# Performance work log

Hardware: AMD Instinct MI355X
Metric: run time of the kernel (lower is better)

## Reference

```python
import jax, jax.numpy as jnp
import numpy as np

N = 10000; E = 60000; D = 3000; H = 512; L = 128; P = 256
NUM_MASK = 3000  # int(0.3 * N)

def prelu(x, a):
    return jnp.where(x >= 0, x, a * x)

def setup_inputs() -> dict:
    key = jax.random.key(0)
    ks = jax.random.split(key, 32)
    def rn(k, shape, scale=0.02):
        return jax.random.normal(k, shape, jnp.float32) * scale
    inp = {
        'x': jax.random.normal(ks[0], (N, D), jnp.float32),
        'edge_index': jax.random.randint(ks[1], (2, E), 0, N),
        'perm': jax.random.permutation(ks[2], N),
        'shuffle': jax.random.permutation(ks[3], N - NUM_MASK),
        's_W1': rn(ks[4], (D, H)), 's_b1': jnp.zeros((H,), jnp.float32), 's_a': jnp.full((1,), 0.25, jnp.float32),
        's_W2': rn(ks[5], (H, L)), 's_b2': jnp.zeros((L,), jnp.float32),
        't_W1': rn(ks[6], (D, H)), 't_b1': jnp.zeros((H,), jnp.float32), 't_a': jnp.full((1,), 0.25, jnp.float32),
        't_W2': rn(ks[7], (H, L)), 't_b2': jnp.zeros((L,), jnp.float32),
        'p_W1': rn(ks[8], (L, P)), 'p_b1': jnp.zeros((P,), jnp.float32), 'p_a': jnp.full((1,), 0.25, jnp.float32),
        'p_W2': rn(ks[9], (P, L)), 'p_b2': jnp.zeros((L,), jnp.float32),
        'tp_W1': rn(ks[10], (L, P)), 'tp_b1': jnp.zeros((P,), jnp.float32), 'tp_a': jnp.full((1,), 0.25, jnp.float32),
        'tp_W2': rn(ks[11], (P, L)), 'tp_b2': jnp.zeros((L,), jnp.float32),
        'dgi_W': rn(ks[12], (L, L), 0.05),
        'pos_token': rn(ks[13], (1, D)), 'neg_token': rn(ks[14], (1, D)),
        'e2d_W': rn(ks[15], (L, L), 0.05),
        'd_W': rn(ks[16], (L, D)), 'd_b': jnp.zeros((D,), jnp.float32),
    }
    return inp

def reference(x, edge_index, perm, shuffle, s_W1, s_b1, s_a, s_W2, s_b2, t_W1, t_b1, t_a, t_W2, t_b2, p_W1, p_b1, p_a, p_W2, p_b2, tp_W1, tp_b1, tp_a, tp_W2, tp_b2, dgi_W, pos_token, neg_token, e2d_W, d_W, d_b):
    n = x.shape[0]
    # GCN normalization with added self loops (PyG gcn_norm, flow source->target)
    loops = jnp.arange(n)
    src = jnp.concatenate([edge_index[0], loops])
    dst = jnp.concatenate([edge_index[1], loops])
    deg = jax.ops.segment_sum(jnp.ones(dst.shape, x.dtype), dst, n)
    dinv = jnp.where(deg > 0, jax.lax.rsqrt(deg), 0.0)
    enorm = (dinv[src] * dinv[dst])[:, None]  # [E+N, 1]

    def gcn(h, W, b):
        h = h @ W  # transform first, then propagate (PyG GCNConv)
        return jax.ops.segment_sum(h[src] * enorm, dst, n) + b

    # feature masking / corruption (bn=False -> Identity; no dropout at eval)
    mask_nodes = perm[:NUM_MASK]
    keep_nodes = perm[NUM_MASK:]
    use_pos = x.at[mask_nodes].add(pos_token[0])
    use_neg = jnp.zeros_like(x).at[keep_nodes].set(x[keep_nodes][shuffle]).at[mask_nodes].add(neg_token[0])

    # student / teacher two-layer GCN encoders (shared PReLU param per encoder)
    rep_pos = prelu(gcn(prelu(gcn(use_pos, s_W1, s_b1), s_a), s_W2, s_b2), s_a)
    rep_neg = prelu(gcn(prelu(gcn(use_neg, t_W1, t_b1), t_a), t_W2, t_b2), t_a)

    def proj(z, W1, b1, a, W2, b2):
        return prelu(z @ W1 + b1, a) @ W2 + b2

    pos_z = proj(rep_pos[mask_nodes], p_W1, p_b1, p_a, p_W2, p_b2)
    neg_z = proj(rep_neg[mask_nodes], tp_W1, tp_b1, tp_a, tp_W2, tp_b2)

    # DGI loss with sigmoid summary of positive embeddings
    s = jax.nn.sigmoid(pos_z.mean(axis=0))  # [L]
    ws = dgi_W @ s
    pos_d = jax.nn.sigmoid(pos_z @ ws)
    neg_d = jax.nn.sigmoid(neg_z @ ws)
    dgi_loss = -jnp.log(pos_d + 1e-15).mean() - jnp.log(1.0 - neg_d + 1e-15).mean()

    # reconstruction: re-mask latent, single-GCN feature decoder (no activation)
    rec = (rep_pos @ e2d_W).at[mask_nodes].set(0.0)
    rec = gcn(rec, d_W, d_b)

    # SCE loss with alpha = 2
    def l2n(v):
        return v / jnp.maximum(jnp.linalg.norm(v, axis=-1, keepdims=True), 1e-12)
    cos = (l2n(x[mask_nodes]) * l2n(rec[mask_nodes])).sum(axis=-1)
    feat_loss = ((1.0 - cos) ** 2).mean()
    return (feat_loss, dgi_loss)
```

## Files before the change

### kernel.cpp

```cpp
#include <hip/hip_runtime.h>

#define NND 10000
#define EE  60000
#define DD  3000
#define HH  512
#define LL  128
#define PP  256
#define NM  3000

#define KP  3072
#define MP  10240
#define NW  1024
#define KTILES (KP/64)

#define BMT 320
#define BNT 128
#define AH_STR 10240
#define AB_STR 20480
#define BH_STR 4096
#define BB_STR 8192

typedef short bf16x8 __attribute__((ext_vector_type(8)));
typedef float f32x4 __attribute__((ext_vector_type(4)));

__device__ __align__(256) char g_ws[(size_t)176 << 20];

__device__ __forceinline__ unsigned short f2b(float f){
    unsigned int x = __float_as_uint(f);
    unsigned int r = x + 0x7FFFu + ((x >> 16) & 1u);
    return (unsigned short)(r >> 16);
}
__device__ __forceinline__ float b2f(unsigned short u){
    return __uint_as_float(((unsigned int)u) << 16);
}
__device__ __forceinline__ float2 bpair(unsigned int u){
    float2 r;
    r.x = __uint_as_float(u << 16);
    r.y = __uint_as_float(u & 0xffff0000u);
    return r;
}
__device__ __forceinline__ unsigned int packb(float a, float b){
    return (unsigned int)f2b(a) | ((unsigned int)f2b(b) << 16);
}

__device__ __forceinline__ void gl_lds16(const void* g, void* l){
    __builtin_amdgcn_global_load_lds(
        (const __attribute__((address_space(1))) unsigned int*)g,
        (__attribute__((address_space(3))) unsigned int*)l, 16, 0, 0);
}


__global__ void init_k(int* degi, int* cursor, float* scal,
                       float* ptW, float* ntW, float* svecraw, int* ecnt){
    int i = blockIdx.x*256 + threadIdx.x;
    if (i < NND){ degi[i]=0; cursor[i]=0; }
    if (i < 80) scal[i]=0.f;
    if (i == 0) ecnt[0]=0;
    if (i < 128) svecraw[i]=0.f;
    if (i < HH){ ptW[i]=0.f; ntW[i]=0.f; }
}

__global__ void count_k(const int* __restrict__ ei, int* degi){
    int i = blockIdx.x*256 + threadIdx.x;
    if (i < EE) atomicAdd(&degi[ei[EE + i]], 1);
}

__global__ void flag_k(const int* __restrict__ perm, const int* __restrict__ shuf,
                       int* flag, int* negsrc){
    int i = blockIdx.x*256 + threadIdx.x;
    if (i < NND){
        int p = perm[i];
        if (i < NM){ flag[p] = 1; negsrc[p] = -1; }
        else       { flag[p] = 0; negsrc[p] = perm[NM + shuf[i - NM]]; }
    }
}

__global__ __launch_bounds__(256) void alloc_k(const int* __restrict__ degi,
                                               float* dinv, int* rowptr, int* ecnt){
    __shared__ int sb[256];
    __shared__ int bbase;
    int t = threadIdx.x;
    int i = blockIdx.x*256 + t;
    int v = (i < NND) ? degi[i] : 0;
    sb[t] = v;
    __syncthreads();
    for (int off = 1; off < 256; off <<= 1){
        int x = 0;
        if (t >= off) x = sb[t - off];
        __syncthreads();
        sb[t] += x;
        __syncthreads();
    }
    if (t == 255) bbase = atomicAdd(ecnt, sb[255]);
    __syncthreads();
    if (i < NND){
        rowptr[i] = bbase + sb[t] - v;
        dinv[i] = 1.f/sqrtf((float)(degi[i] + 1));
    }
}

__global__ void fill_k(const int* __restrict__ ei, const int* __restrict__ rowptr,
                       int* cursor, int* adj){
    int i = blockIdx.x*256 + threadIdx.x;
    if (i < EE){
        int d = ei[EE + i];
        int s = ei[i];
        int p = atomicAdd(&cursor[d], 1);
        adj[rowptr[d] + p] = s;
    }
}

__global__ __launch_bounds__(512) void tok_k(const float* __restrict__ posT,
        const float* __restrict__ negT,
        const float* __restrict__ sW1, const float* __restrict__ tW1,
        float* ptW, float* ntW){
    int b = blockIdx.x; int chunk = blockIdx.y; int j = threadIdx.x;
    const float* tok = b ? negT : posT;
    const float* Wm  = b ? tW1  : sW1;
    float acc = 0.f;
    int d0 = chunk * (DD/8), d1 = d0 + (DD/8);
    for (int d = d0; d < d1; ++d) acc += tok[d] * Wm[(long)d*HH + j];
    atomicAdd(&((b ? ntW : ptW)[j]), acc);
}


__global__ __launch_bounds__(256) void cast_pad_x_k(const float* __restrict__ x,
                                                    unsigned short* __restrict__ xb){
    long idx = (long)blockIdx.x*256 + threadIdx.x;
    if (idx >= (long)MP*(KP/8)) return;
    int row = (int)(idx / (KP/8));
    int g   = (int)(idx % (KP/8));
    unsigned short o[8] = {0,0,0,0,0,0,0,0};
    if (row < NND && g < DD/8){
        const float* src = x + (long)row*DD + g*8;
        float4 a = *(const float4*)(src);
        float4 b = *(const float4*)(src + 4);
        o[0]=f2b(a.x); o[1]=f2b(a.y); o[2]=f2b(a.z); o[3]=f2b(a.w);
        o[4]=f2b(b.x); o[5]=f2b(b.y); o[6]=f2b(b.z); o[7]=f2b(b.w);
    }
    *(uint4*)(xb + (long)row*KP + g*8) = *(const uint4*)o;
}

struct TBatch {
    const float* in[10];
    unsigned short* out[10];
    int R[10], C[10], OS[10];
    int t0[11];
};

__global__ void transbatch_k(TBatch tb){
    __shared__ unsigned short tile[32][33];
    int b = blockIdx.x;
    int d = 0;
    while (d < 9 && b >= tb.t0[d+1]) d++;
    const float* in = tb.in[d];
    unsigned short* out = tb.out[d];
    int R = tb.R[d], C = tb.C[d], OS = tb.OS[d];
    int lt = b - tb.t0[d];
    int Ctiles = (C + 31) >> 5;
    int rt = lt / Ctiles, ct = lt % Ctiles;
    int rb = rt*32, cb = ct*32;
    int tx = threadIdx.x, ty = threadIdx.y;
    for (int i = ty; i < 32; i += 8){
        int r = rb + i, c = cb + tx;
        tile[i][tx] = (r < R && c < C) ? f2b(in[(long)r*C + c]) : (unsigned short)0;
    }
    __syncthreads();
    for (int i = ty; i < 32; i += 8){
        int c = cb + i, r = rb + tx;
        if (c < C && r < OS) out[(long)c*OS + r] = (r < R) ? tile[tx][i] : (unsigned short)0;
    }
}


#define LDA(PB, MT, KS) (*(const bf16x8*)&As[(PB) + (KS)*AH_STR + a_off + (MT)*512])
#define LDB(PB, NT, KS) (*(const bf16x8*)&Bs[(PB) + (KS)*BH_STR + b_off + (NT)*512])

#define STG_A(KT, PDST, P) gl_lds16(asrc[P] + ((KT)<<6), &As[(PDST) + adst[P]])
#define STG_B(KT, PDST, Q) gl_lds16(bsrc[Q] + ((KT)<<6), &Bs[(PDST) + bdst[Q]])

#define GATE7 asm volatile("s_waitcnt vmcnt(7)" ::: "memory")
#define GATE0 asm volatile("s_waitcnt vmcnt(0)" ::: "memory")
#define NOOPS ((void)0)
#define AFENCE asm volatile("" ::: "memory")
#define BARR  { AFENCE; __builtin_amdgcn_s_barrier(); AFENCE; }

#define TILE_BODY(S1_STMT, S2_STMT, GATE_STMT) {                                  \
    bf16x8 af_[5][2], bf_[4][2];                                                  \
    _Pragma("unroll") for (int nt = 0; nt < 4; ++nt){                             \
        bf_[nt][0] = LDB(pB, nt, 0); bf_[nt][1] = LDB(pB, nt, 1); }               \
    _Pragma("unroll") for (int mt = 0; mt < 5; ++mt){                             \
        af_[mt][0] = LDA(pA, mt, 0); af_[mt][1] = LDA(pA, mt, 1); }               \
    S1_STMT;                                                                      \
    BARR;                                                                         \
    __builtin_amdgcn_s_setprio(1);                                                \
    _Pragma("unroll") for (int ks = 0; ks < 2; ++ks)                              \
      _Pragma("unroll") for (int nt = 0; nt < 4; ++nt)                            \
        _Pragma("unroll") for (int mt = 0; mt < 2; ++mt)                          \
          acc[mt][nt] = __builtin_amdgcn_mfma_f32_16x16x32_bf16(af_[mt][ks], bf_[nt][ks], acc[mt][nt], 0,0,0); \
    __builtin_amdgcn_s_setprio(0);                                                \
    BARR;                                                                         \
    S2_STMT;                                                                      \
    __builtin_amdgcn_s_setprio(1);                                                \
    _Pragma("unroll") for (int ks = 0; ks < 2; ++ks)                              \
      _Pragma("unroll") for (int nt = 0; nt < 4; ++nt)                            \
        _Pragma("unroll") for (int mt = 2; mt < 5; ++mt)                          \
          acc[mt][nt] = __builtin_amdgcn_mfma_f32_16x16x32_bf16(af_[mt][ks], bf_[nt][ks], acc[mt][nt], 0,0,0); \
    __builtin_amdgcn_s_setprio(0);                                                \
    GATE_STMT;                                                                    \
    BARR;                                                                         \
}

__global__ __launch_bounds__(512, 2) void gemm320(
    const unsigned short* __restrict__ Ag,
    const unsigned short* __restrict__ Bg,
    unsigned short* __restrict__ C,
    int M, int Cstride)
{
    __shared__ __align__(1024) unsigned short As[3*AB_STR];
    __shared__ __align__(1024) unsigned short Bs[2*BB_STR];

    const int bid = blockIdx.x;
    const int swz = (bid & 7)*32 + (bid >> 3);
    const int m0 = (swz >> 3) * BMT;
    const int n0 = (swz & 7) * BNT;

    const int tid = threadIdx.x;
    const int w   = tid >> 6,  l = tid & 63;
    const int wm  = w >> 1,    wn = w & 1;
    const int l16 = l & 15,    quad = l >> 4;

    const int schunk = (l & 3) ^ (((l >> 5) & 1) << 1);
    const int rq8   = ((quad ^ (((l16 >> 3) & 1) << 1)) << 3);
    const int a_off = ((wm*80 + l16) << 5) + rq8;
    const int b_off = ((wn*64 + l16) << 5) + rq8;

    const unsigned short* asrc[5]; int adst[5];
    #pragma unroll
    for (int p = 0; p < 5; ++p){
        int j = 5*w + p, kh = j/20, g = j - kh*20;
        asrc[p] = Ag + (long)(m0 + g*16 + (l >> 2))*KP + (kh << 5) + (schunk << 3);
        adst[p] = kh*AH_STR + g*512;
    }
    const unsigned short* bsrc[2]; int bdst[2];
    #pragma unroll
    for (int q = 0; q < 2; ++q){
        int j = 2*w + q, kh = j >> 3, g = j & 7;
        bsrc[q] = Bg + (long)(n0 + g*16 + (l >> 2))*KP + (kh << 5) + (schunk << 3);
        bdst[q] = kh*BH_STR + g*512;
    }

    f32x4 acc[5][4];
    #pragma unroll
    for (int i = 0; i < 5; ++i)
        #pragma unroll
        for (int j = 0; j < 4; ++j)
            #pragma unroll
            for (int r = 0; r < 4; ++r) acc[i][j][r] = 0.f;

    #pragma unroll
    for (int p = 0; p < 5; ++p) STG_A(0, 0, p);
    #pragma unroll
    for (int q = 0; q < 2; ++q) STG_B(0, 0, q);
    #pragma unroll
    for (int p = 0; p < 5; ++p) STG_A(1, AB_STR, p);
    #pragma unroll
    for (int q = 0; q < 2; ++q) STG_B(1, BB_STR, q);
    GATE7;
    BARR;

    int ab = 0, bb = 0;
    #pragma unroll 1
    for (int t = 0; t < KTILES-2; ++t){
        const int pA  = ab*AB_STR;
        const int pB  = bb*BB_STR;
        const int ab2 = (ab == 0) ? 2 : ab - 1;
        const int pA2 = ab2*AB_STR;
        TILE_BODY({ STG_A(t+2,pA2,0); STG_A(t+2,pA2,1); STG_A(t+2,pA2,2); STG_A(t+2,pA2,3); },
                  { STG_A(t+2,pA2,4); STG_B(t+2,pB,0); STG_B(t+2,pB,1); },
                  GATE7)
        ab = (ab == 2) ? 0 : ab + 1;
        bb ^= 1;
    }
    {
        const int pA = ab*AB_STR, pB = bb*BB_STR;
        TILE_BODY(NOOPS, NOOPS, GATE0)
        ab = (ab == 2) ? 0 : ab + 1;
        bb ^= 1;
    }
    {
        const int pA = ab*AB_STR, pB = bb*BB_STR;
        TILE_BODY(NOOPS, NOOPS, NOOPS)
    }

    #pragma unroll
    for (int mt = 0; mt < 5; ++mt){
        const int rowb = m0 + wm*80 + mt*16 + quad*4;
        #pragma unroll
        for (int nt = 0; nt < 4; ++nt){
            const int col = n0 + wn*64 + nt*16 + l16;
            #pragma unroll
            for (int r = 0; r < 4; ++r){
                const int row = rowb + r;
                if (row < M) C[(long)row*Cstride + col] = f2b(acc[mt][nt][r]);
            }
        }
    }
}

__device__ __forceinline__ void gemm_bt_body(
    const unsigned short* __restrict__ A,
    const unsigned short* __restrict__ BT,
    void* __restrict__ Cv,
    int M, int Nn, int K, int Cstride,
    const float* __restrict__ bias,
    const float* __restrict__ alpha,
    int epi, const int* __restrict__ ridx, int obf)
{
    __shared__ __align__(16) unsigned short As[64*40];
    __shared__ __align__(16) unsigned short Bs[64*40];
    const int m0 = blockIdx.y*64, n0 = blockIdx.x*64;
    const int t = threadIdx.x;
    const int lrow = t >> 2, lk = (t & 3) * 8;
    const int wave = t >> 6, lane = t & 63;
    const int quad = lane >> 4, l16 = lane & 15;
    f32x4 acc[4];
    #pragma unroll
    for (int i = 0; i < 4; i++)
        for (int j = 0; j < 4; j++) acc[i][j] = 0.f;

    const bool arv = (m0 + lrow) < M;
    const bool brv = (n0 + lrow) < Nn;
    long arow = 0;
    if (arv) arow = ridx ? (long)ridx[m0 + lrow] : (long)(m0 + lrow);
    const long arowbase = arow * K;
    const long browbase = (long)(n0 + lrow) * K;

    for (int k0 = 0; k0 < K; k0 += 32){
        int gk = k0 + lk;
        uint4 av = {0u,0u,0u,0u};
        uint4 bv = {0u,0u,0u,0u};
        if (arv) av = *(const uint4*)(A + arowbase + gk);
        if (brv) bv = *(const uint4*)(BT + browbase + gk);
        *(uint4*)(&As[lrow*40 + lk]) = av;
        *(uint4*)(&Bs[lrow*40 + lk]) = bv;
        __syncthreads();
        bf16x8 af = *(const bf16x8*)(&As[(wave*16 + l16)*40 + quad*8]);
        #pragma unroll
        for (int nt = 0; nt < 4; nt++){
            bf16x8 bfr = *(const bf16x8*)(&Bs[(nt*16 + l16)*40 + quad*8]);
            acc[nt] = __builtin_amdgcn_mfma_f32_16x16x32_bf16(af, bfr, acc[nt], 0, 0, 0);
        }
        __syncthreads();
    }

    const int rowb = m0 + wave*16 + quad*4;
    float aval = (epi == 2) ? alpha[0] : 0.f;
    #pragma unroll
    for (int nt = 0; nt < 4; nt++){
        int col = n0 + nt*16 + l16;
        if (col >= Nn) continue;
        float bvv = epi ? bias[col] : 0.f;
        #pragma unroll
        for (int r = 0; r < 4; r++){
            int row = rowb + r;
            if (row < M){
                float v = acc[nt][r] + bvv;
                if (epi == 2 && v < 0.f) v *= aval;
                if (obf) ((unsigned short*)Cv)[(long)row*Cstride + col] = f2b(v);
                else     ((float*)Cv)[(long)row*Cstride + col] = v;
            }
        }
    }
}

__global__ __launch_bounds__(256) void gemm_bt_ex(
    const unsigned short* __restrict__ A,
    const unsigned short* __restrict__ BT,
    void* __restrict__ Cv,
    int M, int Nn, int K, int Cstride,
    const float* __restrict__ bias,
    const float* __restrict__ alpha,
    int epi, const int* __restrict__ ridx, int obf)
{
    gemm_bt_body(A, BT, Cv, M, Nn, K, Cstride, bias, alpha, epi, ridx, obf);
}

__global__ __launch_bounds__(256) void gemm_bt2(
    const unsigned short* __restrict__ A0, const unsigned short* __restrict__ A1,
    const unsigned short* __restrict__ B0, const unsigned short* __restrict__ B1,
    void* __restrict__ C0, void* __restrict__ C1,
    int M, int Nn, int K, int Cstride,
    const float* __restrict__ bias0, const float* __restrict__ bias1,
    const float* __restrict__ al0, const float* __restrict__ al1,
    int epi, const int* __restrict__ ridx, int obf)
{
    if (blockIdx.z == 0)
        gemm_bt_body(A0, B0, C0, M, Nn, K, Cstride, bias0, al0, epi, ridx, obf);
    else
        gemm_bt_body(A1, B1, C1, M, Nn, K, Cstride, bias1, al1, epi, ridx, obf);
}


__global__ __launch_bounds__(256) void agg1_k(const unsigned short* __restrict__ XW,
    const float* __restrict__ ptW, const float* __restrict__ ntW,
    const int* __restrict__ flag, const int* __restrict__ negsrc,
    const float* __restrict__ dinv, const int* __restrict__ rowptr,
    const int* __restrict__ degi, const int* __restrict__ adj,
    const float* __restrict__ sb1, const float* __restrict__ sav,
    const float* __restrict__ tb1, const float* __restrict__ tav,
    unsigned short* __restrict__ H1p, unsigned short* __restrict__ H1n)
{
    int i = blockIdx.x; int t = threadIdx.x;
    int c = 2*t;
    float di = dinv[i];
    int rs = rowptr[i], re = rs + degi[i];
    float p0 = ptW[c], p1 = ptW[c+1];
    float n0v = ntW[c], n1v = ntW[c+1];
    int fi = flag[i];
    int nsi = negsrc[i]; if (nsi < 0) nsi = 0;
    float ffi = fi ? 1.f : 0.f;
    float2 xp = bpair(*(const unsigned int*)(XW + (long)i*1024 + c));
    float2 xn = bpair(*(const unsigned int*)(XW + (long)nsi*1024 + 512 + c));
    float pa0 = (xp.x + ffi*p0) * di;
    float pa1 = (xp.y + ffi*p1) * di;
    float na0 = (fi ? n0v : xn.x) * di;
    float na1 = (fi ? n1v : xn.y) * di;
    for (int e = rs; e < re; ++e){
        int s = adj[e]; float ds = dinv[s];
        int fs = flag[s];
        int ns = negsrc[s]; if (ns < 0) ns = 0;
        float ffs = fs ? 1.f : 0.f;
        float2 sp = bpair(*(const unsigned int*)(XW + (long)s*1024 + c));
        float2 sn = bpair(*(const unsigned int*)(XW + (long)ns*1024 + 512 + c));
        pa0 += (sp.x + ffs*p0) * ds;
        pa1 += (sp.y + ffs*p1) * ds;
        na0 += (fs ? n0v : sn.x) * ds;
        na1 += (fs ? n1v : sn.y) * ds;
    }
    float sa_ = sav[0], ta_ = tav[0];
    float v0 = di*pa0 + sb1[c];   if (v0 < 0.f) v0 *= sa_;
    float v1 = di*pa1 + sb1[c+1]; if (v1 < 0.f) v1 *= sa_;
    float w0 = di*na0 + tb1[c];   if (w0 < 0.f) w0 *= ta_;
    float w1 = di*na1 + tb1[c+1]; if (w1 < 0.f) w1 *= ta_;
    *(unsigned int*)(H1p + (long)i*512 + c) = packb(v0, v1);
    *(unsigned int*)(H1n + (long)i*512 + c) = packb(w0, w1);
}

__global__ __launch_bounds__(128) void agg128_k(const unsigned short* __restrict__ In,
    const float* __restrict__ dinv, const int* __restrict__ rowptr,
    const int* __restrict__ degi, const int* __restrict__ adj,
    const float* __restrict__ b2, const float* __restrict__ a2,
    unsigned short* __restrict__ Out)
{
    int i = blockIdx.x, t = threadIdx.x;
    float di = dinv[i];
    int rs = rowptr[i], re = rs + degi[i];
    float acc = b2f(In[(long)i*128 + t]) * di;
    for (int e = rs; e < re; ++e){
        int s = adj[e];
        acc += b2f(In[(long)s*128 + t]) * dinv[s];
    }
    float v = di*acc + b2[t];
    float a = a2[0]; if (v < 0.f) v *= a;
    Out[(long)i*128 + t] = f2b(v);
}

__global__ __launch_bounds__(128) void aggrec_k(const unsigned short* __restrict__ recPre,
    const float* __restrict__ dinv, const int* __restrict__ rowptr,
    const int* __restrict__ degi, const int* __restrict__ adj,
    const int* __restrict__ flag, const int* __restrict__ perm,
    unsigned short* __restrict__ recAgg)
{
    int b = blockIdx.x, t = threadIdx.x;
    int i = perm[b];
    float di = dinv[i];
    int rs = rowptr[i], re = rs + degi[i];
    float acc = 0.f;
    for (int e = rs; e < re; ++e){
        int s = adj[e];
        if (!flag[s]) acc += b2f(recPre[(long)s*128 + t]) * dinv[s];
    }
    recAgg[(long)b*128 + t] = f2b(di * acc);
}


__global__ __launch_bounds__(128) void meanp_k(const float* __restrict__ posZ,
                                               float* svecraw){
    int j = threadIdx.x;
    int r0 = blockIdx.x*64, r1 = r0 + 64; if (r1 > NM) r1 = NM;
    float s = 0.f;
    for (int r = r0; r < r1; ++r) s += posZ[(long)r*128 + j];
    atomicAdd(&svecraw[j], s);
}

__global__ void ws_k(const float* __restrict__ dgiW, const float* __restrict__ svecraw,
                     float* wsv){
    __shared__ float s[128];
    int i = threadIdx.x;
    s[i] = 1.f/(1.f + expf(-svecraw[i]/(float)NM));
    __syncthreads();
    float a = 0.f;
    for (int j = 0; j < 128; ++j) a += dgiW[i*128 + j] * s[j];
    wsv[i] = a;
}

__global__ __launch_bounds__(256) void dgi_k(const float* __restrict__ posZ,
    const float* __restrict__ negZ, const float* __restrict__ wsv, float* scal){
    __shared__ float sp[4], sn[4];
    int wid = threadIdx.x >> 6, lane = threadIdx.x & 63;
    float w0 = wsv[lane], w1 = wsv[64 + lane];
    float accp = 0.f, accn = 0.f;
    for (int row = blockIdx.x*4 + wid; row < 2*NM; row += gridDim.x*4){
        const float* Z = (row < NM) ? posZ : negZ;
        int r = (row < NM) ? row : row - NM;
        float v = Z[(long)r*128 + lane] * w0 + Z[(long)r*128 + 64 + lane] * w1;
        for (int off = 32; off; off >>= 1) v += __shfl_down(v, off, 64);
        if (lane == 0){
            float d = 1.f/(1.f + expf(-v));
            if (row < NM) accp += logf(d + 1e-15f);
            else          accn += logf(1.f - d + 1e-15f);
        }
    }
    if (lane == 0){ sp[wid] = accp; sn[wid] = accn; }
    __syncthreads();
    if (threadIdx.x == 0){
        atomicAdd(&scal[0], sp[0]+sp[1]+sp[2]+sp[3]);
        atomicAdd(&scal[1], sn[0]+sn[1]+sn[2]+sn[3]);
    }
}


__global__ __launch_bounds__(256) void cos_k(const float* __restrict__ x,
    const unsigned short* __restrict__ recMask, const int* __restrict__ perm,
    float* scal){
    int b = blockIdx.x, t = threadIdx.x;
    long xi = (long)perm[b]*DD;
    long ri = (long)b*DD;
    float dot = 0.f, nx = 0.f, nr = 0.f;
    for (int d = t; d < DD; d += 256){
        float xv = x[xi + d], rv = b2f(recMask[ri + d]);
        dot += xv*rv; nx += xv*xv; nr += rv*rv;
    }
    for (int off = 32; off; off >>= 1){
        dot += __shfl_down(dot, off, 64);
        nx  += __shfl_down(nx,  off, 64);
        nr  += __shfl_down(nr,  off, 64);
    }
    __shared__ float sd[4], sx[4], sr[4];
    int w = t >> 6, lane = t & 63;
    if (lane == 0){ sd[w] = dot; sx[w] = nx; sr[w] = nr; }
    __syncthreads();
    if (t == 0){
        float Dv = sd[0]+sd[1]+sd[2]+sd[3];
        float Xv = sx[0]+sx[1]+sx[2]+sx[3];
        float Rv = sr[0]+sr[1]+sr[2]+sr[3];
        float c = Dv/(fmaxf(sqrtf(Xv),1e-12f)*fmaxf(sqrtf(Rv),1e-12f));
        float e = 1.f - c;
        atomicAdd(&scal[16 + (b & 63)], e*e);
    }
}

__global__ void fin_k(const float* __restrict__ scal, float* out){
    float fs = 0.f;
    for (int i = 0; i < 64; ++i) fs += scal[16 + i];
    float feat = fs/(float)NM;
    float dgi  = -(scal[0]/(float)NM) - (scal[1]/(float)NM);
    out[0] = feat;
    out[1] = dgi;
}


extern "C" void kernel_launch(void* const* d_in, const int* in_sizes, int n_in,
                              void* d_out, int out_size, void* d_ws, size_t ws_size,
                              hipStream_t stream) {
    (void)in_sizes; (void)n_in; (void)out_size; (void)d_ws; (void)ws_size;
    const float* x  = (const float*)d_in[0];
    const int* ei   = (const int*)d_in[1];
    const int* perm = (const int*)d_in[2];
    const int* shuf = (const int*)d_in[3];
    const float* sW1 = (const float*)d_in[4];
    const float* sb1 = (const float*)d_in[5];
    const float* sa  = (const float*)d_in[6];
    const float* sW2 = (const float*)d_in[7];
    const float* sb2 = (const float*)d_in[8];
    const float* tW1 = (const float*)d_in[9];
    const float* tb1 = (const float*)d_in[10];
    const float* ta  = (const float*)d_in[11];
    const float* tW2 = (const float*)d_in[12];
    const float* tb2 = (const float*)d_in[13];
    const float* pW1 = (const float*)d_in[14];
    const float* pb1 = (const float*)d_in[15];
    const float* pa  = (const float*)d_in[16];
    const float* pW2 = (const float*)d_in[17];
    const float* pb2 = (const float*)d_in[18];
    const float* tpW1 = (const float*)d_in[19];
    const float* tpb1 = (const float*)d_in[20];
    const float* tpa  = (const float*)d_in[21];
    const float* tpW2 = (const float*)d_in[22];
    const float* tpb2 = (const float*)d_in[23];
    const float* dgiW = (const float*)d_in[24];
    const float* posT = (const float*)d_in[25];
    const float* negT = (const float*)d_in[26];
    const float* e2dW = (const float*)d_in[27];
    const float* dW   = (const float*)d_in[28];
    const float* db   = (const float*)d_in[29];
    float* out = (float*)d_out;

    void* wsp = nullptr;
    hipGetSymbolAddress(&wsp, HIP_SYMBOL(g_ws));
    char* base = (char*)wsp;
    size_t off = 0;
    auto alloc = [&](size_t b){ size_t o = off; off = (off + b + 255) & ~(size_t)255; return o; };

    float* dinv    = (float*)(base + alloc(NND*4));
    int* degi      = (int*)  (base + alloc(NND*4));
    int* rowptr    = (int*)  (base + alloc(NND*4));
    int* cursor    = (int*)  (base + alloc(NND*4));
    int* adj       = (int*)  (base + alloc(EE*4));
    int* flag      = (int*)  (base + alloc(NND*4));
    int* negsrc    = (int*)  (base + alloc(NND*4));
    int* ecnt      = (int*)  (base + alloc(16*4));
    float* ptW     = (float*)(base + alloc(HH*4));
    float* ntW     = (float*)(base + alloc(HH*4));
    float* svecraw = (float*)(base + alloc(128*4));
    float* wsv     = (float*)(base + alloc(128*4));
    float* scal    = (float*)(base + alloc(80*4));

    unsigned short* xb    = (unsigned short*)(base + alloc((size_t)MP*KP*2));
    unsigned short* W1T   = (unsigned short*)(base + alloc((size_t)NW*KP*2));
    unsigned short* sW2T  = (unsigned short*)(base + alloc((size_t)LL*HH*2));
    unsigned short* tW2T  = (unsigned short*)(base + alloc((size_t)LL*HH*2));
    unsigned short* pW1T  = (unsigned short*)(base + alloc((size_t)PP*LL*2));
    unsigned short* pW2T  = (unsigned short*)(base + alloc((size_t)LL*PP*2));
    unsigned short* tpW1T = (unsigned short*)(base + alloc((size_t)PP*LL*2));
    unsigned short* tpW2T = (unsigned short*)(base + alloc((size_t)LL*PP*2));
    unsigned short* e2dWT = (unsigned short*)(base + alloc((size_t)LL*LL*2));
    unsigned short* dWT   = (unsigned short*)(base + alloc((size_t)DD*LL*2));

    unsigned short* XW      = (unsigned short*)(base + alloc((size_t)NND*1024*2));
    unsigned short* H1p     = (unsigned short*)(base + alloc((size_t)NND*512*2));
    unsigned short* H1n     = (unsigned short*)(base + alloc((size_t)NND*512*2));
    unsigned short* M2p     = (unsigned short*)(base + alloc((size_t)NND*128*2));
    unsigned short* M2n     = (unsigned short*)(base + alloc((size_t)NND*128*2));
    unsigned short* repP    = (unsigned short*)(base + alloc((size_t)NND*128*2));
    unsigned short* repN    = (unsigned short*)(base + alloc((size_t)NND*128*2));
    unsigned short* posH    = (unsigned short*)(base + alloc((size_t)NM*256*2));
    unsigned short* negH    = (unsigned short*)(base + alloc((size_t)NM*256*2));
    float* posZ             = (float*)(base + alloc((size_t)NM*128*4));
    float* negZ             = (float*)(base + alloc((size_t)NM*128*4));
    unsigned short* recPre  = (unsigned short*)(base + alloc((size_t)NND*128*2));
    unsigned short* recAgg  = (unsigned short*)(base + alloc((size_t)NM*128*2));
    unsigned short* recMask = (unsigned short*)(base + alloc((size_t)NM*DD*2));

    init_k<<<(NND+255)/256, 256, 0, stream>>>(degi, cursor, scal, ptW, ntW, svecraw, ecnt);
    flag_k<<<(NND+255)/256, 256, 0, stream>>>(perm, shuf, flag, negsrc);
    count_k<<<(EE+255)/256, 256, 0, stream>>>(ei, degi);
    alloc_k<<<(NND+255)/256, 256, 0, stream>>>(degi, dinv, rowptr, ecnt);
    fill_k<<<(EE+255)/256, 256, 0, stream>>>(ei, rowptr, cursor, adj);
    tok_k<<<dim3(2,8), 512, 0, stream>>>(posT, negT, sW1, tW1, ptW, ntW);

    cast_pad_x_k<<<(int)(((long)MP*(KP/8) + 255)/256), 256, 0, stream>>>(x, xb);
    {
        TBatch tb;
        const float* ins[10] = {sW1, tW1, sW2, tW2, pW1, pW2, tpW1, tpW2, e2dW, dW};
        unsigned short* outs[10] = {W1T, W1T + (size_t)HH*KP, sW2T, tW2T, pW1T, pW2T,
                                    tpW1T, tpW2T, e2dWT, dWT};
        int Rs[10]  = {DD, DD, HH, HH, LL, PP, LL, PP, LL, LL};
        int Cs[10]  = {HH, HH, LL, LL, PP, LL, PP, LL, LL, DD};
        int OSs[10] = {KP, KP, HH, HH, LL, PP, LL, PP, LL, LL};
        int cum = 0;
        for (int d = 0; d < 10; d++){
            tb.in[d] = ins[d]; tb.out[d] = outs[d];
            tb.R[d] = Rs[d]; tb.C[d] = Cs[d]; tb.OS[d] = OSs[d];
            tb.t0[d] = cum;
            cum += (OSs[d]/32) * ((Cs[d] + 31)/32);
        }
        tb.t0[10] = cum;
        transbatch_k<<<cum, dim3(32,8), 0, stream>>>(tb);
    }

    gemm320<<<256, 512, 0, stream>>>(xb, W1T, XW, NND, 1024);
    agg1_k<<<NND, 256, 0, stream>>>(XW, ptW, ntW, flag, negsrc, dinv, rowptr, degi, adj,
                                    sb1, sa, tb1, ta, H1p, H1n);

    gemm_bt2<<<dim3(2,157,2), 256, 0, stream>>>(H1p, H1n, sW2T, tW2T, M2p, M2n,
                                                NND, LL, HH, LL,
                                                nullptr, nullptr, nullptr, nullptr,
                                                0, nullptr, 1);
    agg128_k<<<NND, 128, 0, stream>>>(M2p, dinv, rowptr, degi, adj, sb2, sa, repP);
    agg128_k<<<NND, 128, 0, stream>>>(M2n, dinv, rowptr, degi, adj, tb2, ta, repN);

    gemm_bt2<<<dim3(4,47,2), 256, 0, stream>>>(repP, repN, pW1T, tpW1T, posH, negH,
                                               NM, PP, LL, PP,
                                               pb1, tpb1, pa, tpa, 2, perm, 1);
    gemm_bt2<<<dim3(2,47,2), 256, 0, stream>>>(posH, negH, pW2T, tpW2T, posZ, negZ,
                                               NM, LL, PP, LL,
                                               pb2, tpb2, nullptr, nullptr, 1, nullptr, 0);

    meanp_k<<<47, 128, 0, stream>>>(posZ, svecraw);
    ws_k<<<1, 128, 0, stream>>>(dgiW, svecraw, wsv);
    dgi_k<<<128, 256, 0, stream>>>(posZ, negZ, wsv, scal);

    gemm_bt_ex<<<dim3(2,157), 256, 0, stream>>>(repP, e2dWT, recPre, NND, LL, LL, LL,
                                                nullptr, nullptr, 0, nullptr, 1);
    aggrec_k<<<NM, 128, 0, stream>>>(recPre, dinv, rowptr, degi, adj, flag, perm, recAgg);
    gemm_bt_ex<<<dim3(47,47), 256, 0, stream>>>(recAgg, dWT, recMask, NM, DD, LL, DD,
                                                db, nullptr, 1, nullptr, 1);
    cos_k<<<NM, 256, 0, stream>>>(x, recMask, perm, scal);

    fin_k<<<1, 1, 0, stream>>>(scal, out);
}
```

Before: 524.0 us.

## Batch small kernel launches and drop a barrier in the GEMM tile loop

Merges degree counting with mask flag construction, fuses the two second-layer aggregations into one 2D launch, and batches the projector first layer with the e2d GEMM into a single three-way grid. The token projection is split across 64 chunks instead of 8 for more parallelism. One workgroup barrier in the main GEMM tile body is removed to cut sync stalls, which risks an LDS read/write race if buffers overlap.

```diff
diff --git a/kernel.cpp b/kernel.cpp
--- a/kernel.cpp
+++ b/kernel.cpp
@@ -60,14 +60,11 @@
     if (i < HH){ ptW[i]=0.f; ntW[i]=0.f; }
 }
 
-__global__ void count_k(const int* __restrict__ ei, int* degi){
+__global__ void build_k(const int* __restrict__ ei,
+                        const int* __restrict__ perm, const int* __restrict__ shuf,
+                        int* degi, int* flag, int* negsrc){
     int i = blockIdx.x*256 + threadIdx.x;
     if (i < EE) atomicAdd(&degi[ei[EE + i]], 1);
-}
-
-__global__ void flag_k(const int* __restrict__ perm, const int* __restrict__ shuf,
-                       int* flag, int* negsrc){
-    int i = blockIdx.x*256 + threadIdx.x;
     if (i < NND){
         int p = perm[i];
         if (i < NM){ flag[p] = 1; negsrc[p] = -1; }
@@ -118,7 +115,7 @@
     const float* tok = b ? negT : posT;
     const float* Wm  = b ? tW1  : sW1;
     float acc = 0.f;
-    int d0 = chunk * (DD/8), d1 = d0 + (DD/8);
+    int d0 = chunk * 47, d1 = d0 + 47; if (d1 > DD) d1 = DD;
     for (int d = d0; d < d1; ++d) acc += tok[d] * Wm[(long)d*HH + j];
     atomicAdd(&((b ? ntW : ptW)[j]), acc);
 }
@@ -192,7 +189,6 @@
     _Pragma("unroll") for (int mt = 0; mt < 5; ++mt){                             \
         af_[mt][0] = LDA(pA, mt, 0); af_[mt][1] = LDA(pA, mt, 1); }               \
     S1_STMT;                                                                      \
-    BARR;                                                                         \
     __builtin_amdgcn_s_setprio(1);                                                \
     _Pragma("unroll") for (int ks = 0; ks < 2; ++ks)                              \
       _Pragma("unroll") for (int nt = 0; nt < 4; ++nt)                            \
@@ -399,6 +395,29 @@
         gemm_bt_body(A0, B0, C0, M, Nn, K, Cstride, bias0, al0, epi, ridx, obf);
     else
         gemm_bt_body(A1, B1, C1, M, Nn, K, Cstride, bias1, al1, epi, ridx, obf);
+}
+
+__global__ __launch_bounds__(256) void gemm_bt3(
+    const unsigned short* __restrict__ repP, const unsigned short* __restrict__ repN,
+    const unsigned short* __restrict__ pW1T, const unsigned short* __restrict__ tpW1T,
+    const unsigned short* __restrict__ e2dWT,
+    unsigned short* __restrict__ posH, unsigned short* __restrict__ negH,
+    unsigned short* __restrict__ recPre,
+    const float* __restrict__ pb1, const float* __restrict__ tpb1,
+    const float* __restrict__ pa, const float* __restrict__ tpa,
+    const int* __restrict__ perm)
+{
+    int z = blockIdx.z;
+    if (z == 0){
+        if (blockIdx.y < 47)
+            gemm_bt_body(repP, pW1T, posH, NM, PP, LL, PP, pb1, pa, 2, perm, 1);
+    } else if (z == 1){
+        if (blockIdx.y < 47)
+            gemm_bt_body(repN, tpW1T, negH, NM, PP, LL, PP, tpb1, tpa, 2, perm, 1);
+    } else {
+        if (blockIdx.x < 2)
+            gemm_bt_body(repP, e2dWT, recPre, NND, LL, LL, LL, nullptr, nullptr, 0, nullptr, 1);
+    }
 }
 
 
@@ -447,13 +466,20 @@
     *(unsigned int*)(H1n + (long)i*512 + c) = packb(w0, w1);
 }
 
-__global__ __launch_bounds__(128) void agg128_k(const unsigned short* __restrict__ In,
+__global__ __launch_bounds__(128) void agg128_k(
+    const unsigned short* __restrict__ In0, const unsigned short* __restrict__ In1,
     const float* __restrict__ dinv, const int* __restrict__ rowptr,
     const int* __restrict__ degi, const int* __restrict__ adj,
-    const float* __restrict__ b2, const float* __restrict__ a2,
-    unsigned short* __restrict__ Out)
+    const float* __restrict__ b20, const float* __restrict__ b21,
+    const float* __restrict__ a20, const float* __restrict__ a21,
+    unsigned short* __restrict__ Out0, unsigned short* __restrict__ Out1)
 {
     int i = blockIdx.x, t = threadIdx.x;
+    int h = blockIdx.y;
+    const unsigned short* In = h ? In1 : In0;
+    const float* b2 = h ? b21 : b20;
+    const float* a2 = h ? a21 : a20;
+    unsigned short* Out = h ? Out1 : Out0;
     float di = dinv[i];
     int rs = rowptr[i], re = rs + degi[i];
     float acc = b2f(In[(long)i*128 + t]) * di;
@@ -654,11 +680,10 @@
     unsigned short* recMask = (unsigned short*)(base + alloc((size_t)NM*DD*2));
 
     init_k<<<(NND+255)/256, 256, 0, stream>>>(degi, cursor, scal, ptW, ntW, svecraw, ecnt);
-    flag_k<<<(NND+255)/256, 256, 0, stream>>>(perm, shuf, flag, negsrc);
-    count_k<<<(EE+255)/256, 256, 0, stream>>>(ei, degi);
+    build_k<<<(EE+255)/256, 256, 0, stream>>>(ei, perm, shuf, degi, flag, negsrc);
     alloc_k<<<(NND+255)/256, 256, 0, stream>>>(degi, dinv, rowptr, ecnt);
     fill_k<<<(EE+255)/256, 256, 0, stream>>>(ei, rowptr, cursor, adj);
-    tok_k<<<dim3(2,8), 512, 0, stream>>>(posT, negT, sW1, tW1, ptW, ntW);
+    tok_k<<<dim3(2,64), 512, 0, stream>>>(posT, negT, sW1, tW1, ptW, ntW);
 
     cast_pad_x_k<<<(int)(((long)MP*(KP/8) + 255)/256), 256, 0, stream>>>(x, xb);
     {
@@ -688,25 +713,24 @@
                                                 NND, LL, HH, LL,
                                                 nullptr, nullptr, nullptr, nullptr,
                                                 0, nullptr, 1);
-    agg128_k<<<NND, 128, 0, stream>>>(M2p, dinv, rowptr, degi, adj, sb2, sa, repP);
-    agg128_k<<<NND, 128, 0, stream>>>(M2n, dinv, rowptr, degi, adj, tb2, ta, repN);
-
-    gemm_bt2<<<dim3(4,47,2), 256, 0, stream>>>(repP, repN, pW1T, tpW1T, posH, negH,
-                                               NM, PP, LL, PP,
-                                               pb1, tpb1, pa, tpa, 2, perm, 1);
+    agg128_k<<<dim3(NND,2), 128, 0, stream>>>(M2p, M2n, dinv, rowptr, degi, adj,
+                                              sb2, tb2, sa, ta, repP, repN);
+
+    gemm_bt3<<<dim3(4,157,3), 256, 0, stream>>>(repP, repN, pW1T, tpW1T, e2dWT,
+                                                posH, negH, recPre,
+                                                pb1, tpb1, pa, tpa, perm);
     gemm_bt2<<<dim3(2,47,2), 256, 0, stream>>>(posH, negH, pW2T, tpW2T, posZ, negZ,
                                                NM, LL, PP, LL,
                                                pb2, tpb2, nullptr, nullptr, 1, nullptr, 0);
 
+    aggrec_k<<<NM, 128, 0, stream>>>(recPre, dinv, rowptr, degi, adj, flag, perm, recAgg);
+    gemm_bt_ex<<<dim3(47,47), 256, 0, stream>>>(recAgg, dWT, recMask, NM, DD, LL, DD,
+                                                db, nullptr, 1, nullptr, 1);
+
     meanp_k<<<47, 128, 0, stream>>>(posZ, svecraw);
     ws_k<<<1, 128, 0, stream>>>(dgiW, svecraw, wsv);
     dgi_k<<<128, 256, 0, stream>>>(posZ, negZ, wsv, scal);
 
-    gemm_bt_ex<<<dim3(2,157), 256, 0, stream>>>(repP, e2dWT, recPre, NND, LL, LL, LL,
-                                                nullptr, nullptr, 0, nullptr, 1);
-    aggrec_k<<<NM, 128, 0, stream>>>(recPre, dinv, rowptr, degi, adj, flag, perm, recAgg);
-    gemm_bt_ex<<<dim3(47,47), 256, 0, stream>>>(recAgg, dWT, recMask, NM, DD, LL, DD,
-                                                db, nullptr, 1, nullptr, 1);
     cos_k<<<NM, 256, 0, stream>>>(x, recMask, perm, scal);
 
     fin_k<<<1, 1, 0, stream>>>(scal, out);
```

Result: faster. 509.6 us (-2.7%).
